# Kernel optimization log

Measured on AMD Instinct MI355X. Metric: run time of the kernel, lower is better.

The kernel has to match this reference:

```python
import jax, jax.numpy as jnp
import numpy as np

E, T, H, I = 8, 1024, 2048, 4096  # experts, tokens/expert, hidden, intermediate


def setup_inputs() -> dict:
    key = jax.random.key(0)
    k1, k2, k3, k4, k5 = jax.random.split(key, 5)
    x = jax.random.normal(k1, (E, T, H), dtype=jnp.float32)
    # is_transposed=True layout: [E, H, 2I] and [E, I, H]
    gate_up_proj = jax.random.normal(k2, (E, H, 2 * I), dtype=jnp.float32)
    down_proj = jax.random.normal(k3, (E, I, H), dtype=jnp.float32)
    gate_up_proj_bias = jax.random.normal(k4, (E, 2 * I), dtype=jnp.float32)
    down_proj_bias = jax.random.normal(k5, (E, H), dtype=jnp.float32)
    return {
        "x": x,
        "gate_up_proj": gate_up_proj,
        "gate_up_proj_bias": gate_up_proj_bias,
        "down_proj": down_proj,
        "down_proj_bias": down_proj_bias,
    }


def reference(x, gate_up_proj, gate_up_proj_bias, down_proj, down_proj_bias):
    # grouped GEMM: per-expert x[e] @ gate_up_proj[e] + bias  -> [E, T, 2I]
    gu = jnp.einsum("eth,eho->eto", x, gate_up_proj) + gate_up_proj_bias[:, None, :]
    gate, up = jnp.split(gu, 2, axis=-1)  # SwiGLU
    hidden = jax.nn.silu(gate) * up  # [E, T, I]
    out = jnp.einsum("eti,eih->eth", hidden, down_proj) + down_proj_bias[:, None, :]
    return out
```

## Files before the change

kernel.cpp:

```cpp
#include <hip/hip_runtime.h>


#define E_ 8
#define T_ 1024
#define H_ 2048
#define I_ 4096

typedef unsigned short ushort_t;
typedef unsigned int uint_t;
typedef float f32x4 __attribute__((ext_vector_type(4)));
typedef __bf16 bf16x8 __attribute__((ext_vector_type(8)));
typedef unsigned short ushort8 __attribute__((ext_vector_type(8)));

__device__ inline ushort_t f2bf(float f) {
  uint_t u = __float_as_uint(f);
  u += 0x7fffu + ((u >> 16) & 1u);
  return (ushort_t)(u >> 16);
}
__device__ inline float bf2f(ushort_t h) {
  return __uint_as_float(((uint_t)h) << 16);
}

__device__ inline void async_copy16(void* lds, const void* gptr) {
  __builtin_amdgcn_global_load_lds(
      (__attribute__((address_space(1))) void*)(void*)gptr,
      (__attribute__((address_space(3))) void*)lds,
      16, 0, 0);
}

__global__ __launch_bounds__(256) void cvt_kernel(const float* __restrict__ in,
                                                  ushort_t* __restrict__ out) {
  size_t base = (size_t)(blockIdx.x * 256 + threadIdx.x) * 8;
  f32x4 a = *(const f32x4*)(in + base);
  f32x4 b = *(const f32x4*)(in + base + 4);
  ushort8 o;
  o[0] = f2bf(a[0]); o[1] = f2bf(a[1]); o[2] = f2bf(a[2]); o[3] = f2bf(a[3]);
  o[4] = f2bf(b[0]); o[5] = f2bf(b[1]); o[6] = f2bf(b[2]); o[7] = f2bf(b[3]);
  *(ushort8*)(out + base) = o;
}

__global__ __launch_bounds__(256) void transpose_kernel(
    const float* __restrict__ in, ushort_t* __restrict__ out, int R, int C) {
  __shared__ float tile[64][33];
  const int e = blockIdx.z;
  const float* inb = in + (size_t)e * R * C;
  ushort_t* outb = out + (size_t)e * R * C;
  const int c0 = blockIdx.x * 32, r0 = blockIdx.y * 64;
  const int tx = threadIdx.x, ty = threadIdx.y;
#pragma unroll
  for (int jr = 0; jr < 8; ++jr) {
    int row = ty + 8 * jr;
    tile[row][tx] = inb[(size_t)(r0 + row) * C + c0 + tx];
  }
  __syncthreads();
#pragma unroll
  for (int jo = 0; jo < 4; ++jo) {
    int cc = ty + 8 * jo;
    int rr = 2 * tx;
    ushort2 v;
    v.x = f2bf(tile[rr][cc]);
    v.y = f2bf(tile[rr + 1][cc]);
    *(ushort2*)&outb[(size_t)(c0 + cc) * R + r0 + rr] = v;
  }
}

#define BM 128
#define BN 128
#define BK 64

template <bool OUT_BF16>
__global__ __launch_bounds__(256) void gemm_kernel(
    const ushort_t* __restrict__ A, const ushort_t* __restrict__ B,
    const float* __restrict__ bias, void* __restrict__ Cout,
    int M, int N, int K, int lda) {
  __shared__ ushort_t As[BM * BK];
  __shared__ ushort_t Bs[BN * BK];
  const int e = blockIdx.z;
  const ushort_t* Ab = A + (size_t)e * M * lda;
  const ushort_t* Bb = B + (size_t)e * N * K;
  const float* biasb = bias + (size_t)e * N;
  const int m0 = blockIdx.y * BM;
  const int n0 = blockIdx.x * BN;
  const int tid = threadIdx.x;
  const int wv = tid >> 6, lane = tid & 63;
  const int wm = (wv >> 1) * 64, wn = (wv & 1) * 64;
  const int quad = lane >> 4, lr = lane & 15;

  f32x4 acc[4][4] = {};

  for (int k0 = 0; k0 < K; k0 += BK) {
#pragma unroll
    for (int r = 0; r < 4; ++r) {
      int chunk = r * 256 + tid;
      int row = chunk >> 3;
      int kc = (chunk & 7) * 8;
      async_copy16(&As[chunk * 8], &Ab[(size_t)(m0 + row) * lda + k0 + kc]);
      async_copy16(&Bs[chunk * 8], &Bb[(size_t)(n0 + row) * K + k0 + kc]);
    }
    __syncthreads();
#pragma unroll
    for (int ks = 0; ks < 2; ++ks) {
      bf16x8 af[4], bfr[4];
#pragma unroll
      for (int i = 0; i < 4; ++i)
        af[i] = *(const bf16x8*)&As[(wm + 16 * i + lr) * BK + ks * 32 + quad * 8];
#pragma unroll
      for (int j = 0; j < 4; ++j)
        bfr[j] = *(const bf16x8*)&Bs[(wn + 16 * j + lr) * BK + ks * 32 + quad * 8];
#pragma unroll
      for (int i = 0; i < 4; ++i)
#pragma unroll
        for (int j = 0; j < 4; ++j)
          acc[i][j] = __builtin_amdgcn_mfma_f32_16x16x32_bf16(
              af[i], bfr[j], acc[i][j], 0, 0, 0);
    }
    __syncthreads();
  }

  ushort_t* Cb16 = (ushort_t*)Cout + (size_t)e * M * N;
  float* Cb32 = (float*)Cout + (size_t)e * M * N;
#pragma unroll
  for (int j = 0; j < 4; ++j) {
    int col = n0 + wn + 16 * j + lr;
    float bv = biasb[col];
#pragma unroll
    for (int i = 0; i < 4; ++i) {
      int rowb = m0 + wm + 16 * i + quad * 4;
#pragma unroll
      for (int r = 0; r < 4; ++r) {
        float v = acc[i][j][r] + bv;
        if constexpr (OUT_BF16)
          Cb16[(size_t)(rowb + r) * N + col] = f2bf(v);
        else
          Cb32[(size_t)(rowb + r) * N + col] = v;
      }
    }
  }
}

__global__ __launch_bounds__(256) void silu_kernel(ushort_t* __restrict__ gu) {
  size_t gid = (size_t)blockIdx.x * 256 + threadIdx.x;
  size_t base = gid * 8;
  size_t row = base >> 12;
  int ic = (int)(base & (I_ - 1));
  ushort_t* p = gu + row * (2 * I_) + ic;
  ushort8 g8 = *(const ushort8*)p;
  ushort8 u8 = *(const ushort8*)(p + I_);
  ushort8 h;
#pragma unroll
  for (int r = 0; r < 8; ++r) {
    float g = bf2f(g8[r]);
    float u = bf2f(u8[r]);
    float s = g / (1.0f + __expf(-g));
    h[r] = f2bf(s * u);
  }
  *(ushort8*)p = h;
}

extern "C" void kernel_launch(void* const* d_in, const int* in_sizes, int n_in,
                              void* d_out, int out_size, void* d_ws, size_t ws_size,
                              hipStream_t stream) {
  const float* x   = (const float*)d_in[0];
  const float* wgu = (const float*)d_in[1];
  const float* bgu = (const float*)d_in[2];
  const float* wd  = (const float*)d_in[3];
  const float* bd  = (const float*)d_in[4];
  float* out = (float*)d_out;

  char* ws = (char*)d_ws;
  ushort_t* xb    = (ushort_t*)(ws);
  ushort_t* wgu_t = (ushort_t*)(ws + 33554432);
  ushort_t* wd_t  = (ushort_t*)(ws + 33554432 + 268435456);
  ushort_t* gu    = (ushort_t*)(ws + 33554432 + 268435456 + 134217728);

  cvt_kernel<<<8192, 256, 0, stream>>>(x, xb);
  transpose_kernel<<<dim3(2 * I_ / 32, H_ / 64, E_), dim3(32, 8), 0, stream>>>(
      wgu, wgu_t, H_, 2 * I_);
  transpose_kernel<<<dim3(H_ / 32, I_ / 64, E_), dim3(32, 8), 0, stream>>>(
      wd, wd_t, I_, H_);
  gemm_kernel<true><<<dim3(2 * I_ / BN, T_ / BM, E_), 256, 0, stream>>>(
      xb, wgu_t, bgu, gu, T_, 2 * I_, H_, H_);
  silu_kernel<<<16384, 256, 0, stream>>>(gu);
  gemm_kernel<false><<<dim3(H_ / BN, T_ / BM, E_), 256, 0, stream>>>(
      gu, wd_t, bd, out, T_, H_, I_, 2 * I_);
}
```

Measured before the change: 1.672 ms.

## Fuse SwiGLU into first GEMM, swizzle LDS tiles, vectorize weight transpose

The first GEMM now loads matching gate and up weight tiles and applies bias, SiLU and the product in its epilogue. It writes a compact [T, I] hidden buffer, so the separate silu kernel and the round trip of the 2I-wide intermediate through memory go away. Both GEMMs now use an XOR swizzle on the LDS k-chunks to reduce bank conflicts on fragment reads. The transpose kernel uses 64x64 tiles with float4 loads, an XOR-swizzled tile and 16-byte bf16 stores.

```diff
diff --git a/kernel.cpp b/kernel.cpp
--- a/kernel.cpp
+++ b/kernel.cpp
@@ -17,15 +17,16 @@
   u += 0x7fffu + ((u >> 16) & 1u);
   return (ushort_t)(u >> 16);
 }
-__device__ inline float bf2f(ushort_t h) {
-  return __uint_as_float(((uint_t)h) << 16);
-}
 
 __device__ inline void async_copy16(void* lds, const void* gptr) {
   __builtin_amdgcn_global_load_lds(
       (__attribute__((address_space(1))) void*)(void*)gptr,
       (__attribute__((address_space(3))) void*)lds,
       16, 0, 0);
+}
+
+__device__ inline int swz_kc(int chunk) {
+  return ((chunk & 7) ^ ((chunk >> 3) & 7)) * 8;
 }
 
 __global__ __launch_bounds__(256) void cvt_kernel(const float* __restrict__ in,
@@ -41,46 +42,129 @@
 
 __global__ __launch_bounds__(256) void transpose_kernel(
     const float* __restrict__ in, ushort_t* __restrict__ out, int R, int C) {
-  __shared__ float tile[64][33];
+  __shared__ float tile[64 * 64];
   const int e = blockIdx.z;
   const float* inb = in + (size_t)e * R * C;
   ushort_t* outb = out + (size_t)e * R * C;
-  const int c0 = blockIdx.x * 32, r0 = blockIdx.y * 64;
-  const int tx = threadIdx.x, ty = threadIdx.y;
-#pragma unroll
-  for (int jr = 0; jr < 8; ++jr) {
-    int row = ty + 8 * jr;
-    tile[row][tx] = inb[(size_t)(r0 + row) * C + c0 + tx];
+  const int c0 = blockIdx.x * 64, r0 = blockIdx.y * 64;
+  const int t = threadIdx.x;
+  const int lrow = t >> 4, lc4 = t & 15;
+#pragma unroll
+  for (int rr = 0; rr < 64; rr += 16) {
+    int r = lrow + rr;
+    f32x4 v = *(const f32x4*)&inb[(size_t)(r0 + r) * C + c0 + lc4 * 4];
+    *(f32x4*)&tile[r * 64 + 4 * (lc4 ^ (r >> 3))] = v;
   }
   __syncthreads();
-#pragma unroll
-  for (int jo = 0; jo < 4; ++jo) {
-    int cc = ty + 8 * jo;
-    int rr = 2 * tx;
-    ushort2 v;
-    v.x = f2bf(tile[rr][cc]);
-    v.y = f2bf(tile[rr + 1][cc]);
-    *(ushort2*)&outb[(size_t)(c0 + cc) * R + r0 + rr] = v;
-  }
-}
-
-#define BM 128
-#define BN 128
-#define BK 64
-
-template <bool OUT_BF16>
-__global__ __launch_bounds__(256) void gemm_kernel(
+  const int oc = t >> 3, orr = (t & 7) * 8;
+#pragma unroll
+  for (int cc = 0; cc < 64; cc += 32) {
+    int c = oc + cc;
+    ushort8 o;
+#pragma unroll
+    for (int k = 0; k < 8; ++k) {
+      int r = orr + k;
+      o[k] = f2bf(tile[r * 64 + 4 * ((c >> 2) ^ (r >> 3)) + (c & 3)]);
+    }
+    *(ushort8*)&outb[(size_t)(c0 + c) * R + r0 + orr] = o;
+  }
+}
+
+#define G_BK 64
+
+__global__ __launch_bounds__(256) void gemm1_swiglu_kernel(
     const ushort_t* __restrict__ A, const ushort_t* __restrict__ B,
-    const float* __restrict__ bias, void* __restrict__ Cout,
-    int M, int N, int K, int lda) {
-  __shared__ ushort_t As[BM * BK];
-  __shared__ ushort_t Bs[BN * BK];
+    const float* __restrict__ bias, ushort_t* __restrict__ Hd) {
+  __shared__ ushort_t As[128 * G_BK];
+  __shared__ ushort_t Bg[64 * G_BK];
+  __shared__ ushort_t Bu[64 * G_BK];
   const int e = blockIdx.z;
-  const ushort_t* Ab = A + (size_t)e * M * lda;
-  const ushort_t* Bb = B + (size_t)e * N * K;
-  const float* biasb = bias + (size_t)e * N;
-  const int m0 = blockIdx.y * BM;
-  const int n0 = blockIdx.x * BN;
+  const ushort_t* Ab = A + (size_t)e * T_ * H_;
+  const ushort_t* Bb = B + (size_t)e * (2 * I_) * H_;
+  const float* biasb = bias + (size_t)e * 2 * I_;
+  const int m0 = blockIdx.y * 128;
+  const int n0 = blockIdx.x * 64;
+  const int tid = threadIdx.x;
+  const int wv = tid >> 6, lane = tid & 63;
+  const int wm = (wv >> 1) * 64, wn = (wv & 1) * 32;
+  const int quad = lane >> 4, lr = lane & 15;
+
+  f32x4 accg[4][2] = {};
+  f32x4 accu[4][2] = {};
+
+  for (int k0 = 0; k0 < H_; k0 += G_BK) {
+#pragma unroll
+    for (int r = 0; r < 4; ++r) {
+      int chunk = r * 256 + tid;
+      int row = chunk >> 3;
+      async_copy16(&As[chunk * 8],
+                   &Ab[(size_t)(m0 + row) * H_ + k0 + swz_kc(chunk)]);
+    }
+#pragma unroll
+    for (int r = 0; r < 2; ++r) {
+      int chunk = r * 256 + tid;
+      int row = chunk >> 3;
+      int kc = k0 + swz_kc(chunk);
+      async_copy16(&Bg[chunk * 8], &Bb[(size_t)(n0 + row) * H_ + kc]);
+      async_copy16(&Bu[chunk * 8], &Bb[(size_t)(I_ + n0 + row) * H_ + kc]);
+    }
+    __syncthreads();
+#pragma unroll
+    for (int ks = 0; ks < 2; ++ks) {
+      const int sw = ((ks * 4 + quad) ^ (lr & 7)) * 8;
+      bf16x8 af[4], bg[2], bu[2];
+#pragma unroll
+      for (int i = 0; i < 4; ++i)
+        af[i] = *(const bf16x8*)&As[(wm + 16 * i + lr) * G_BK + sw];
+#pragma unroll
+      for (int j = 0; j < 2; ++j) {
+        bg[j] = *(const bf16x8*)&Bg[(wn + 16 * j + lr) * G_BK + sw];
+        bu[j] = *(const bf16x8*)&Bu[(wn + 16 * j + lr) * G_BK + sw];
+      }
+#pragma unroll
+      for (int i = 0; i < 4; ++i)
+#pragma unroll
+        for (int j = 0; j < 2; ++j) {
+          accg[i][j] = __builtin_amdgcn_mfma_f32_16x16x32_bf16(
+              af[i], bg[j], accg[i][j], 0, 0, 0);
+          accu[i][j] = __builtin_amdgcn_mfma_f32_16x16x32_bf16(
+              af[i], bu[j], accu[i][j], 0, 0, 0);
+        }
+    }
+    __syncthreads();
+  }
+
+  ushort_t* Hb = Hd + (size_t)e * T_ * I_;
+#pragma unroll
+  for (int j = 0; j < 2; ++j) {
+    int col = n0 + wn + 16 * j + lr;
+    float bgv = biasb[col];
+    float buv = biasb[I_ + col];
+#pragma unroll
+    for (int i = 0; i < 4; ++i) {
+      int rowb = m0 + wm + 16 * i + quad * 4;
+#pragma unroll
+      for (int r = 0; r < 4; ++r) {
+        float g = accg[i][j][r] + bgv;
+        float u = accu[i][j][r] + buv;
+        float s = g / (1.0f + __expf(-g));
+        Hb[(size_t)(rowb + r) * I_ + col] = f2bf(s * u);
+      }
+    }
+  }
+}
+
+__global__ __launch_bounds__(256) void gemm2_kernel(
+    const ushort_t* __restrict__ A, const ushort_t* __restrict__ B,
+    const float* __restrict__ bias, float* __restrict__ C) {
+  __shared__ ushort_t As[128 * G_BK];
+  __shared__ ushort_t Bs[128 * G_BK];
+  const int e = blockIdx.z;
+  const ushort_t* Ab = A + (size_t)e * T_ * I_;
+  const ushort_t* Bb = B + (size_t)e * H_ * I_;
+  const float* biasb = bias + (size_t)e * H_;
+  const int m0 = blockIdx.y * 128;
+  const int n0 = blockIdx.x * 128;
   const int tid = threadIdx.x;
   const int wv = tid >> 6, lane = tid & 63;
   const int wm = (wv >> 1) * 64, wn = (wv & 1) * 64;
@@ -88,25 +172,26 @@
 
   f32x4 acc[4][4] = {};
 
-  for (int k0 = 0; k0 < K; k0 += BK) {
+  for (int k0 = 0; k0 < I_; k0 += G_BK) {
 #pragma unroll
     for (int r = 0; r < 4; ++r) {
       int chunk = r * 256 + tid;
       int row = chunk >> 3;
-      int kc = (chunk & 7) * 8;
-      async_copy16(&As[chunk * 8], &Ab[(size_t)(m0 + row) * lda + k0 + kc]);
-      async_copy16(&Bs[chunk * 8], &Bb[(size_t)(n0 + row) * K + k0 + kc]);
+      int kc = k0 + swz_kc(chunk);
+      async_copy16(&As[chunk * 8], &Ab[(size_t)(m0 + row) * I_ + kc]);
+      async_copy16(&Bs[chunk * 8], &Bb[(size_t)(n0 + row) * I_ + kc]);
     }
     __syncthreads();
 #pragma unroll
     for (int ks = 0; ks < 2; ++ks) {
+      const int sw = ((ks * 4 + quad) ^ (lr & 7)) * 8;
       bf16x8 af[4], bfr[4];
 #pragma unroll
       for (int i = 0; i < 4; ++i)
-        af[i] = *(const bf16x8*)&As[(wm + 16 * i + lr) * BK + ks * 32 + quad * 8];
+        af[i] = *(const bf16x8*)&As[(wm + 16 * i + lr) * G_BK + sw];
 #pragma unroll
       for (int j = 0; j < 4; ++j)
-        bfr[j] = *(const bf16x8*)&Bs[(wn + 16 * j + lr) * BK + ks * 32 + quad * 8];
+        bfr[j] = *(const bf16x8*)&Bs[(wn + 16 * j + lr) * G_BK + sw];
 #pragma unroll
       for (int i = 0; i < 4; ++i)
 #pragma unroll
@@ -117,8 +202,7 @@
     __syncthreads();
   }
 
-  ushort_t* Cb16 = (ushort_t*)Cout + (size_t)e * M * N;
-  float* Cb32 = (float*)Cout + (size_t)e * M * N;
+  float* Cb = C + (size_t)e * T_ * H_;
 #pragma unroll
   for (int j = 0; j < 4; ++j) {
     int col = n0 + wn + 16 * j + lr;
@@ -127,34 +211,10 @@
     for (int i = 0; i < 4; ++i) {
       int rowb = m0 + wm + 16 * i + quad * 4;
 #pragma unroll
-      for (int r = 0; r < 4; ++r) {
-        float v = acc[i][j][r] + bv;
-        if constexpr (OUT_BF16)
-          Cb16[(size_t)(rowb + r) * N + col] = f2bf(v);
-        else
-          Cb32[(size_t)(rowb + r) * N + col] = v;
-      }
-    }
-  }
-}
-
-__global__ __launch_bounds__(256) void silu_kernel(ushort_t* __restrict__ gu) {
-  size_t gid = (size_t)blockIdx.x * 256 + threadIdx.x;
-  size_t base = gid * 8;
-  size_t row = base >> 12;
-  int ic = (int)(base & (I_ - 1));
-  ushort_t* p = gu + row * (2 * I_) + ic;
-  ushort8 g8 = *(const ushort8*)p;
-  ushort8 u8 = *(const ushort8*)(p + I_);
-  ushort8 h;
-#pragma unroll
-  for (int r = 0; r < 8; ++r) {
-    float g = bf2f(g8[r]);
-    float u = bf2f(u8[r]);
-    float s = g / (1.0f + __expf(-g));
-    h[r] = f2bf(s * u);
-  }
-  *(ushort8*)p = h;
+      for (int r = 0; r < 4; ++r)
+        Cb[(size_t)(rowb + r) * H_ + col] = acc[i][j][r] + bv;
+    }
+  }
 }
 
 extern "C" void kernel_launch(void* const* d_in, const int* in_sizes, int n_in,
@@ -168,19 +228,18 @@
   float* out = (float*)d_out;
 
   char* ws = (char*)d_ws;
-  ushort_t* xb    = (ushort_t*)(ws);
-  ushort_t* wgu_t = (ushort_t*)(ws + 33554432);
-  ushort_t* wd_t  = (ushort_t*)(ws + 33554432 + 268435456);
-  ushort_t* gu    = (ushort_t*)(ws + 33554432 + 268435456 + 134217728);
+  ushort_t* xb     = (ushort_t*)(ws);
+  ushort_t* wgu_t  = (ushort_t*)(ws + 33554432);
+  ushort_t* wd_t   = (ushort_t*)(ws + 33554432 + 268435456);
+  ushort_t* hidden = (ushort_t*)(ws + 33554432 + 268435456 + 134217728);
 
   cvt_kernel<<<8192, 256, 0, stream>>>(x, xb);
-  transpose_kernel<<<dim3(2 * I_ / 32, H_ / 64, E_), dim3(32, 8), 0, stream>>>(
+  transpose_kernel<<<dim3(2 * I_ / 64, H_ / 64, E_), 256, 0, stream>>>(
       wgu, wgu_t, H_, 2 * I_);
-  transpose_kernel<<<dim3(H_ / 32, I_ / 64, E_), dim3(32, 8), 0, stream>>>(
+  transpose_kernel<<<dim3(H_ / 64, I_ / 64, E_), 256, 0, stream>>>(
       wd, wd_t, I_, H_);
-  gemm_kernel<true><<<dim3(2 * I_ / BN, T_ / BM, E_), 256, 0, stream>>>(
-      xb, wgu_t, bgu, gu, T_, 2 * I_, H_, H_);
-  silu_kernel<<<16384, 256, 0, stream>>>(gu);
-  gemm_kernel<false><<<dim3(H_ / BN, T_ / BM, E_), 256, 0, stream>>>(
-      gu, wd_t, bd, out, T_, H_, I_, 2 * I_);
-}
+  gemm1_swiglu_kernel<<<dim3(I_ / 64, T_ / 128, E_), 256, 0, stream>>>(
+      xb, wgu_t, bgu, hidden);
+  gemm2_kernel<<<dim3(H_ / 128, T_ / 128, E_), 256, 0, stream>>>(
+      hidden, wd_t, bd, out);
+}
```

Result: faster. 1.511 ms (-9.6%).
